# Kernel optimization log

Hardware: AMD Instinct MI355X
Metric: run time of the kernel (lower is better)

## Reference

```python
import jax, jax.numpy as jnp
import numpy as np

B, N, D, H, DK, DV = 16, 512, 512, 8, 64, 64


def setup_inputs() -> dict:
    key = jax.random.key(0)
    ks = jax.random.split(key, 16)
    xav = lambda k, fi, fo: jax.random.uniform(k, (fi, fo), jnp.float32,
                                               -jnp.sqrt(6.0 / (fi + fo)), jnp.sqrt(6.0 / (fi + fo)))
    return {
        "queries": jax.random.normal(ks[0], (B, N, D), jnp.float32),
        "keys": jax.random.normal(ks[1], (B, N, D), jnp.float32),
        "values": jax.random.normal(ks[2], (B, N, D), jnp.float32),
        "box_relation_embed_matrix": jax.random.uniform(ks[3], (B, H, N, N), jnp.float32),
        "ExtrAtt": jax.random.normal(ks[4], (B, H, N, N), jnp.float32),
        "Wq": xav(ks[5], D, H * DK), "bq": jnp.zeros((H * DK,), jnp.float32),
        "Wk": xav(ks[6], D, H * DK), "bk": jnp.zeros((H * DK,), jnp.float32),
        "Wv": xav(ks[7], D, H * DV), "bv": jnp.zeros((H * DV,), jnp.float32),
        "Wo": xav(ks[8], H * DV, D), "bo": jnp.zeros((D,), jnp.float32),
    }


def reference(queries, keys, values, box_relation_embed_matrix, ExtrAtt,
              Wq, bq, Wk, bk, Wv, bv, Wo, bo):
    b_s, nq, _ = queries.shape
    nk = keys.shape[1]
    # projections -> [B, H, N, d]
    q = (queries @ Wq + bq).reshape(b_s, nq, H, DK).transpose(0, 2, 1, 3)
    k = (keys @ Wk + bk).reshape(b_s, nk, H, DK).transpose(0, 2, 1, 3)
    v = (values @ Wv + bv).reshape(b_s, nk, H, DV).transpose(0, 2, 1, 3)
    scale = 1.0 / jnp.sqrt(jnp.asarray(DK, queries.dtype))
    att = jnp.einsum('bhqd,bhkd->bhqk', q, k) * scale
    # log geometric (box) bias + content attention, first softmax
    w_mn = jnp.log(jnp.clip(box_relation_embed_matrix, 1e-6, None)) + att
    w_mn = jax.nn.softmax(w_mn, axis=-1)
    # dropout is identity in eval; add extra attention and re-normalize
    att2 = jax.nn.softmax(w_mn + ExtrAtt, axis=-1)
    out = jnp.einsum('bhqk,bhkd->bhqd', att2, v)
    out = out.transpose(0, 2, 1, 3).reshape(b_s, nq, H * DV)
    return out @ Wo + bo
```

## Files before the change

### kernel.cpp

```cpp
#include <hip/hip_runtime.h>
#include <hip/hip_bf16.h>

#define NB 16
#define NN 512
#define ND 512
#define NH 8

using short8 = __attribute__((ext_vector_type(8))) short;
using f32x4  = __attribute__((ext_vector_type(4))) float;

static __device__ __forceinline__ unsigned short f2bf(float f) {
  unsigned u = __builtin_bit_cast(unsigned, f);
  unsigned r = 0x7fffu + ((u >> 16) & 1u);
  return (unsigned short)((u + r) >> 16);
}
static __device__ __forceinline__ float bf2f(unsigned short u) {
  return __builtin_bit_cast(float, (unsigned)u << 16);
}

__global__ __launch_bounds__(256) void wprep(
    const float* __restrict__ Wq, const float* __restrict__ Wk,
    const float* __restrict__ Wv, const float* __restrict__ Wo,
    unsigned short* __restrict__ T) {
  const float* W;
  switch (blockIdx.z) {
    case 0: W = Wq; break;
    case 1: W = Wk; break;
    case 2: W = Wv; break;
    default: W = Wo; break;
  }
  unsigned short* Wt = T + (size_t)blockIdx.z * 512 * 512;
  __shared__ float tile[64][65];
  const int t = threadIdx.x;
  const int k0 = blockIdx.x * 64, n0 = blockIdx.y * 64;
#pragma unroll
  for (int it = 0; it < 4; ++it) {
    int row = it * 16 + (t >> 4);
    int c4 = (t & 15) * 4;
    float4 v = *(const float4*)&W[(size_t)(k0 + row) * 512 + n0 + c4];
    tile[row][c4] = v.x; tile[row][c4 + 1] = v.y;
    tile[row][c4 + 2] = v.z; tile[row][c4 + 3] = v.w;
  }
  __syncthreads();
#pragma unroll
  for (int it = 0; it < 4; ++it) {
    int nr = it * 16 + (t >> 4);
    int k4 = (t & 15) * 4;
    ushort4 o;
    o.x = f2bf(tile[k4 + 0][nr]); o.y = f2bf(tile[k4 + 1][nr]);
    o.z = f2bf(tile[k4 + 2][nr]); o.w = f2bf(tile[k4 + 3][nr]);
    *(ushort4*)&Wt[(size_t)(n0 + nr) * 512 + k0 + k4] = o;
  }
}

__global__ __launch_bounds__(256) void qkv_gemm(
    const float* __restrict__ Xq, const float* __restrict__ Xk,
    const float* __restrict__ Xv, const unsigned short* __restrict__ Wt,
    const float* __restrict__ bq, const float* __restrict__ bk,
    const float* __restrict__ bv, unsigned short* __restrict__ q_ws,
    unsigned short* __restrict__ k_ws, unsigned short* __restrict__ vt_ws) {
  const int zi = blockIdx.z;
  const float* X = (zi == 0) ? Xq : (zi == 1) ? Xk : Xv;
  const unsigned short* Wz = Wt + (size_t)zi * 512 * 512;
  const float* bias = (zi == 0) ? bq : (zi == 1) ? bk : bv;
  const int m0 = blockIdx.x * 128, n0 = blockIdx.y * 128;
  __shared__ unsigned short Al[2][128][40];
  __shared__ unsigned short Bl[2][128][40];
  const int t = threadIdx.x;
  const int w = t >> 6, l = t & 63;
  const int lr = l & 15, lg = l >> 4;
  const int wr = (w >> 1) * 64, wc = (w & 1) * 64;
  f32x4 acc[4][4] = {};
  for (int kk = 0; kk < 512; kk += 64) {
    __syncthreads();
    {
      const int colk = (t & 15) * 4;
      const int kc = colk >> 5, kin = colk & 31;
#pragma unroll
      for (int p = 0; p < 8; ++p) {
        int row = p * 16 + (t >> 4);
        float4 v = *(const float4*)&X[(size_t)(m0 + row) * 512 + kk + colk];
        ushort4 o;
        o.x = f2bf(v.x); o.y = f2bf(v.y); o.z = f2bf(v.z); o.w = f2bf(v.w);
        *(ushort4*)&Al[kc][row][kin] = o;
      }
      const int colk8 = (t & 7) * 8;
      const int kc2 = colk8 >> 5, kin2 = colk8 & 31;
#pragma unroll
      for (int p = 0; p < 4; ++p) {
        int row = p * 32 + (t >> 3);
        short8 v = *(const short8*)&Wz[(size_t)(n0 + row) * 512 + kk + colk8];
        *(short8*)&Bl[kc2][row][kin2] = v;
      }
    }
    __syncthreads();
#pragma unroll
    for (int kc = 0; kc < 2; ++kc) {
      short8 a[4], b[4];
      const int lk = lg * 8;
#pragma unroll
      for (int i = 0; i < 4; ++i) a[i] = *(const short8*)&Al[kc][wr + i * 16 + lr][lk];
#pragma unroll
      for (int i = 0; i < 4; ++i) b[i] = *(const short8*)&Bl[kc][wc + i * 16 + lr][lk];
#pragma unroll
      for (int i = 0; i < 4; ++i)
#pragma unroll
        for (int j = 0; j < 4; ++j)
          acc[i][j] = __builtin_amdgcn_mfma_f32_16x16x32_bf16(a[i], b[j], acc[i][j], 0, 0, 0);
    }
  }
#pragma unroll
  for (int j = 0; j < 4; ++j) {
    const int col = n0 + wc + j * 16 + lr;
    const float bb = bias[col];
    const int hh = col >> 6, dv = col & 63;
#pragma unroll
    for (int i = 0; i < 4; ++i) {
      const int mbase = m0 + wr + i * 16 + lg * 4;
      const int b_ = mbase >> 9, nt = mbase & 511;
      if (zi == 2) {
        ushort4 o;
        o.x = f2bf(acc[i][j][0] + bb); o.y = f2bf(acc[i][j][1] + bb);
        o.z = f2bf(acc[i][j][2] + bb); o.w = f2bf(acc[i][j][3] + bb);
        *(ushort4*)&vt_ws[((size_t)(b_ * NH + hh) * 64 + dv) * 512 + nt] = o;
      } else {
        unsigned short* dst = (zi == 0) ? q_ws : k_ws;
#pragma unroll
        for (int r = 0; r < 4; ++r)
          dst[((size_t)(b_ * NH + hh) * 512 + nt + r) * 64 + dv] = f2bf(acc[i][j][r] + bb);
      }
    }
  }
}

__global__ __launch_bounds__(256, 8) void attn_kernel(
    const unsigned short* __restrict__ q_ws, const unsigned short* __restrict__ k_ws,
    const unsigned short* __restrict__ vt_ws, const float* __restrict__ box,
    const float* __restrict__ Ext, unsigned short* __restrict__ hidden) {
  const int t = threadIdx.x;
  const int w = t >> 6, l = t & 63;
  const int lr = l & 15, lg = l >> 4;
  const int bh = blockIdx.y;
  const int q0 = blockIdx.x * 16;
  const int b = bh >> 3, h = bh & 7;

  const unsigned short* Qp = q_ws + (size_t)bh * 512 * 64;
  const unsigned short* Kp = k_ws + (size_t)bh * 512 * 64;
  const unsigned short* Vt = vt_ws + (size_t)bh * 64 * 512;
  const float* boxp = box + ((size_t)bh * 512 + q0) * 512;
  const float* Ep = Ext + ((size_t)bh * 512 + q0) * 512;

  __shared__ float red[4][16];
  __shared__ float red2[4][16];
  __shared__ __align__(16) unsigned char wsh[4][4352];

  const int n0w = w * 128;
  unsigned short(*Pw)[136] = (unsigned short(*)[136])wsh[w];

  short8 qf0 = *(const short8*)&Qp[(size_t)(q0 + lr) * 64 + lg * 8];
  short8 qf1 = *(const short8*)&Qp[(size_t)(q0 + lr) * 64 + 32 + lg * 8];

  float s1 = 0.f;
#pragma unroll
  for (int c = 0; c < 8; ++c) {
    const int krow = n0w + c * 16 + lr;
    short8 kf0 = *(const short8*)&Kp[(size_t)krow * 64 + lg * 8];
    short8 kf1 = *(const short8*)&Kp[(size_t)krow * 64 + 32 + lg * 8];
    f32x4 bx4 = *(const f32x4*)&boxp[(size_t)lr * 512 + n0w + c * 16 + lg * 4];
    f32x4 a = {0.f, 0.f, 0.f, 0.f};
    a = __builtin_amdgcn_mfma_f32_16x16x32_bf16(kf0, qf0, a, 0, 0, 0);
    a = __builtin_amdgcn_mfma_f32_16x16x32_bf16(kf1, qf1, a, 0, 0, 0);
    ushort4 o;
    {
      float e0 = fmaxf(bx4[0], 1e-6f) * __expf(a[0] * 0.125f);
      float e1 = fmaxf(bx4[1], 1e-6f) * __expf(a[1] * 0.125f);
      float e2 = fmaxf(bx4[2], 1e-6f) * __expf(a[2] * 0.125f);
      float e3 = fmaxf(bx4[3], 1e-6f) * __expf(a[3] * 0.125f);
      s1 += (e0 + e1) + (e2 + e3);
      o.x = f2bf(e0); o.y = f2bf(e1); o.z = f2bf(e2); o.w = f2bf(e3);
    }
    *(ushort4*)&Pw[lr][c * 16 + lg * 4] = o;
  }
  s1 += __shfl_xor(s1, 16);
  s1 += __shfl_xor(s1, 32);
  if (lg == 0) red[w][lr] = s1;
  __syncthreads();
  const float l1i = 1.0f / (red[0][lr] + red[1][lr] + red[2][lr] + red[3][lr]);

  float s2 = 0.f;
#pragma unroll
  for (int c = 0; c < 8; ++c) {
    f32x4 ex4 = *(const f32x4*)&Ep[(size_t)lr * 512 + n0w + c * 16 + lg * 4];
    ushort4 u = *(const ushort4*)&Pw[lr][c * 16 + lg * 4];
    ushort4 o;
    {
      float e0 = __expf(bf2f(u.x) * l1i + ex4[0]);
      float e1 = __expf(bf2f(u.y) * l1i + ex4[1]);
      float e2 = __expf(bf2f(u.z) * l1i + ex4[2]);
      float e3 = __expf(bf2f(u.w) * l1i + ex4[3]);
      s2 += (e0 + e1) + (e2 + e3);
      o.x = f2bf(e0); o.y = f2bf(e1); o.z = f2bf(e2); o.w = f2bf(e3);
    }
    *(ushort4*)&Pw[lr][c * 16 + lg * 4] = o;
  }
  s2 += __shfl_xor(s2, 16);
  s2 += __shfl_xor(s2, 32);
  if (lg == 0) red2[w][lr] = s2;
  __syncthreads();

  f32x4 o4[4] = {};
#pragma unroll
  for (int kc = 0; kc < 4; ++kc) {
    short8 pa = *(const short8*)&Pw[lr][kc * 32 + lg * 8];
#pragma unroll
    for (int c2 = 0; c2 < 4; ++c2) {
      short8 vf = *(const short8*)&Vt[(size_t)(c2 * 16 + lr) * 512 + n0w + kc * 32 + lg * 8];
      o4[c2] = __builtin_amdgcn_mfma_f32_16x16x32_bf16(pa, vf, o4[c2], 0, 0, 0);
    }
  }
  f32x4 rs = *(const f32x4*)&red2[0][lg * 4];
#pragma unroll
  for (int w2 = 1; w2 < 4; ++w2) {
    f32x4 p = *(const f32x4*)&red2[w2][lg * 4];
#pragma unroll
    for (int r = 0; r < 4; ++r) rs[r] += p[r];
  }
  f32x4 l2v;
#pragma unroll
  for (int r = 0; r < 4; ++r) l2v[r] = 1.0f / rs[r];
  float* ow = (float*)wsh[w];
#pragma unroll
  for (int c2 = 0; c2 < 4; ++c2)
#pragma unroll
    for (int r = 0; r < 4; ++r)
      ow[(lg * 4 + r) * 68 + c2 * 16 + lr] = o4[c2][r] * l2v[r];
  __syncthreads();
  {
    const int lrow = t >> 4;
    const int d4 = (t & 15) * 4;
    f32x4 s = *(const f32x4*)&((const float*)wsh[0])[lrow * 68 + d4];
#pragma unroll
    for (int w2 = 1; w2 < 4; ++w2) {
      f32x4 p = *(const f32x4*)&((const float*)wsh[w2])[lrow * 68 + d4];
#pragma unroll
      for (int r = 0; r < 4; ++r) s[r] += p[r];
    }
    ushort4 oo;
    oo.x = f2bf(s[0]); oo.y = f2bf(s[1]); oo.z = f2bf(s[2]); oo.w = f2bf(s[3]);
    *(ushort4*)&hidden[(size_t)(b * 512 + q0 + lrow) * 512 + h * 64 + d4] = oo;
  }
}

__global__ __launch_bounds__(256) void out_gemm(
    const unsigned short* __restrict__ hidden, const unsigned short* __restrict__ WoT,
    const float* __restrict__ bo, float* __restrict__ out) {
  const int m0 = blockIdx.x * 128, n0 = blockIdx.y * 128;
  __shared__ unsigned short Al[2][128][40];
  __shared__ unsigned short Bl[2][128][40];
  const int t = threadIdx.x;
  const int w = t >> 6, l = t & 63;
  const int lr = l & 15, lg = l >> 4;
  const int wr = (w >> 1) * 64, wc = (w & 1) * 64;
  f32x4 acc[4][4] = {};
  for (int kk = 0; kk < 512; kk += 64) {
    __syncthreads();
    {
      const int colk8 = (t & 7) * 8;
      const int kc2 = colk8 >> 5, kin2 = colk8 & 31;
#pragma unroll
      for (int p = 0; p < 4; ++p) {
        int row = p * 32 + (t >> 3);
        short8 v = *(const short8*)&hidden[(size_t)(m0 + row) * 512 + kk + colk8];
        *(short8*)&Al[kc2][row][kin2] = v;
      }
#pragma unroll
      for (int p = 0; p < 4; ++p) {
        int row = p * 32 + (t >> 3);
        short8 v = *(const short8*)&WoT[(size_t)(n0 + row) * 512 + kk + colk8];
        *(short8*)&Bl[kc2][row][kin2] = v;
      }
    }
    __syncthreads();
#pragma unroll
    for (int kc = 0; kc < 2; ++kc) {
      short8 a[4], b[4];
      const int lk = lg * 8;
#pragma unroll
      for (int i = 0; i < 4; ++i) a[i] = *(const short8*)&Al[kc][wr + i * 16 + lr][lk];
#pragma unroll
      for (int i = 0; i < 4; ++i) b[i] = *(const short8*)&Bl[kc][wc + i * 16 + lr][lk];
#pragma unroll
      for (int i = 0; i < 4; ++i)
#pragma unroll
        for (int j = 0; j < 4; ++j)
          acc[i][j] = __builtin_amdgcn_mfma_f32_16x16x32_bf16(a[i], b[j], acc[i][j], 0, 0, 0);
    }
  }
#pragma unroll
  for (int j = 0; j < 4; ++j) {
    const int col = n0 + wc + j * 16 + lr;
    const float bb = bo[col];
#pragma unroll
    for (int i = 0; i < 4; ++i)
#pragma unroll
      for (int r = 0; r < 4; ++r)
        out[(size_t)(m0 + wr + i * 16 + lg * 4 + r) * 512 + col] = acc[i][j][r] + bb;
  }
}

extern "C" void kernel_launch(void* const* d_in, const int* in_sizes, int n_in,
                              void* d_out, int out_size, void* d_ws, size_t ws_size,
                              hipStream_t stream) {
  const float* queries = (const float*)d_in[0];
  const float* keys = (const float*)d_in[1];
  const float* values = (const float*)d_in[2];
  const float* box = (const float*)d_in[3];
  const float* ext = (const float*)d_in[4];
  const float* Wq = (const float*)d_in[5];
  const float* bq = (const float*)d_in[6];
  const float* Wk = (const float*)d_in[7];
  const float* bk = (const float*)d_in[8];
  const float* Wv = (const float*)d_in[9];
  const float* bv = (const float*)d_in[10];
  const float* Wo = (const float*)d_in[11];
  const float* bo = (const float*)d_in[12];
  float* out = (float*)d_out;

  char* ws = (char*)d_ws;
  unsigned short* q_ws = (unsigned short*)(ws);
  unsigned short* k_ws = (unsigned short*)(ws + 8u * 1024 * 1024);
  unsigned short* vt_ws = (unsigned short*)(ws + 16u * 1024 * 1024);
  unsigned short* hidden = (unsigned short*)(ws + 24u * 1024 * 1024);
  unsigned short* wt = (unsigned short*)(ws + 32u * 1024 * 1024);

  wprep<<<dim3(8, 8, 4), 256, 0, stream>>>(Wq, Wk, Wv, Wo, wt);
  qkv_gemm<<<dim3(64, 4, 3), 256, 0, stream>>>(queries, keys, values, wt, bq, bk, bv,
                                               q_ws, k_ws, vt_ws);
  attn_kernel<<<dim3(32, 128), 256, 0, stream>>>(q_ws, k_ws, vt_ws, box, ext, hidden);
  out_gemm<<<dim3(64, 4), 256, 0, stream>>>(hidden, wt + 3u * 512 * 512, bo, out);
}
```

Measured before the change: 176.5 us.

## Stage box and ExtrAtt tiles into LDS asynchronously, prefetching ExtrAtt during softmax

The attention kernel now copies its box and ExtrAtt tiles from global memory straight into a per-wave, XOR-swizzled LDS buffer with global_load_lds. The ExtrAtt load is issued while the first softmax pass finishes, so its latency overlaps with that compute. All K fragments are loaded up front and the QK MFMAs run before the wait on the box load. Plain __syncthreads is replaced with explicit waitcnt plus s_barrier. In exchange, each block uses roughly 50KB of LDS and launch bounds drop from 8 to 3, so occupancy falls and there is less latency hiding across waves.

```diff
diff --git a/kernel.cpp b/kernel.cpp
--- a/kernel.cpp
+++ b/kernel.cpp
@@ -16,6 +16,10 @@
 }
 static __device__ __forceinline__ float bf2f(unsigned short u) {
   return __builtin_bit_cast(float, (unsigned)u << 16);
+}
+static __device__ __forceinline__ void ld_lds16(const float* g, float* l) {
+  __builtin_amdgcn_global_load_lds((const __attribute__((address_space(1))) void*)g,
+                                   (__attribute__((address_space(3))) void*)l, 16, 0, 0);
 }
 
 __global__ __launch_bounds__(256) void wprep(
@@ -133,7 +137,7 @@
   }
 }
 
-__global__ __launch_bounds__(256, 8) void attn_kernel(
+__global__ __launch_bounds__(256, 3) void attn_kernel(
     const unsigned short* __restrict__ q_ws, const unsigned short* __restrict__ k_ws,
     const unsigned short* __restrict__ vt_ws, const float* __restrict__ box,
     const float* __restrict__ Ext, unsigned short* __restrict__ hidden) {
@@ -150,63 +154,90 @@
   const float* boxp = box + ((size_t)bh * 512 + q0) * 512;
   const float* Ep = Ext + ((size_t)bh * 512 + q0) * 512;
 
+  __shared__ float stg[4][2048];
+  __shared__ unsigned short Pt[4][16][144];
   __shared__ float red[4][16];
   __shared__ float red2[4][16];
-  __shared__ __align__(16) unsigned char wsh[4][4352];
 
   const int n0w = w * 128;
-  unsigned short(*Pw)[136] = (unsigned short(*)[136])wsh[w];
+  float* wst = stg[w];
+  unsigned short(*Pw)[144] = Pt[w];
 
   short8 qf0 = *(const short8*)&Qp[(size_t)(q0 + lr) * 64 + lg * 8];
   short8 qf1 = *(const short8*)&Qp[(size_t)(q0 + lr) * 64 + 32 + lg * 8];
-
-  float s1 = 0.f;
+  short8 kf[8][2];
 #pragma unroll
   for (int c = 0; c < 8; ++c) {
     const int krow = n0w + c * 16 + lr;
-    short8 kf0 = *(const short8*)&Kp[(size_t)krow * 64 + lg * 8];
-    short8 kf1 = *(const short8*)&Kp[(size_t)krow * 64 + 32 + lg * 8];
-    f32x4 bx4 = *(const f32x4*)&boxp[(size_t)lr * 512 + n0w + c * 16 + lg * 4];
+    kf[c][0] = *(const short8*)&Kp[(size_t)krow * 64 + lg * 8];
+    kf[c][1] = *(const short8*)&Kp[(size_t)krow * 64 + 32 + lg * 8];
+  }
+#pragma unroll
+  for (int it = 0; it < 8; ++it) {
+    const int row2 = it * 2 + (l >> 5);
+    const int slot = (l & 31) ^ (row2 & 7);
+    ld_lds16(&boxp[(size_t)row2 * 512 + n0w + slot * 4], &wst[it * 256]);
+  }
+  __builtin_amdgcn_sched_barrier(0);
+
+  f32x4 z[8];
+#pragma unroll
+  for (int c = 0; c < 8; ++c) {
     f32x4 a = {0.f, 0.f, 0.f, 0.f};
-    a = __builtin_amdgcn_mfma_f32_16x16x32_bf16(kf0, qf0, a, 0, 0, 0);
-    a = __builtin_amdgcn_mfma_f32_16x16x32_bf16(kf1, qf1, a, 0, 0, 0);
+    a = __builtin_amdgcn_mfma_f32_16x16x32_bf16(kf[c][0], qf0, a, 0, 0, 0);
+    a = __builtin_amdgcn_mfma_f32_16x16x32_bf16(kf[c][1], qf1, a, 0, 0, 0);
+    z[c] = a;
+  }
+  asm volatile("s_waitcnt vmcnt(0)" ::: "memory");
+
+  float s1 = 0.f;
+#pragma unroll
+  for (int c = 0; c < 8; ++c) {
+    f32x4 bx4 = *(const f32x4*)&wst[lr * 128 + (((c * 4 + lg) ^ (lr & 7)) << 2)];
     ushort4 o;
-    {
-      float e0 = fmaxf(bx4[0], 1e-6f) * __expf(a[0] * 0.125f);
-      float e1 = fmaxf(bx4[1], 1e-6f) * __expf(a[1] * 0.125f);
-      float e2 = fmaxf(bx4[2], 1e-6f) * __expf(a[2] * 0.125f);
-      float e3 = fmaxf(bx4[3], 1e-6f) * __expf(a[3] * 0.125f);
-      s1 += (e0 + e1) + (e2 + e3);
-      o.x = f2bf(e0); o.y = f2bf(e1); o.z = f2bf(e2); o.w = f2bf(e3);
-    }
+    float e0 = fmaxf(bx4[0], 1e-6f) * __expf(z[c][0] * 0.125f);
+    float e1 = fmaxf(bx4[1], 1e-6f) * __expf(z[c][1] * 0.125f);
+    float e2 = fmaxf(bx4[2], 1e-6f) * __expf(z[c][2] * 0.125f);
+    float e3 = fmaxf(bx4[3], 1e-6f) * __expf(z[c][3] * 0.125f);
+    s1 += (e0 + e1) + (e2 + e3);
+    o.x = f2bf(e0); o.y = f2bf(e1); o.z = f2bf(e2); o.w = f2bf(e3);
     *(ushort4*)&Pw[lr][c * 16 + lg * 4] = o;
   }
+  asm volatile("s_waitcnt lgkmcnt(0)" ::: "memory");
+#pragma unroll
+  for (int it = 0; it < 8; ++it) {
+    const int row2 = it * 2 + (l >> 5);
+    const int slot = (l & 31) ^ (row2 & 7);
+    ld_lds16(&Ep[(size_t)row2 * 512 + n0w + slot * 4], &wst[it * 256]);
+  }
+  __builtin_amdgcn_sched_barrier(0);
   s1 += __shfl_xor(s1, 16);
   s1 += __shfl_xor(s1, 32);
   if (lg == 0) red[w][lr] = s1;
-  __syncthreads();
+  asm volatile("s_waitcnt lgkmcnt(0)" ::: "memory");
+  __builtin_amdgcn_s_barrier();
   const float l1i = 1.0f / (red[0][lr] + red[1][lr] + red[2][lr] + red[3][lr]);
+  asm volatile("s_waitcnt vmcnt(0)" ::: "memory");
 
   float s2 = 0.f;
 #pragma unroll
   for (int c = 0; c < 8; ++c) {
-    f32x4 ex4 = *(const f32x4*)&Ep[(size_t)lr * 512 + n0w + c * 16 + lg * 4];
+    f32x4 ex4 = *(const f32x4*)&wst[lr * 128 + (((c * 4 + lg) ^ (lr & 7)) << 2)];
     ushort4 u = *(const ushort4*)&Pw[lr][c * 16 + lg * 4];
     ushort4 o;
-    {
-      float e0 = __expf(bf2f(u.x) * l1i + ex4[0]);
-      float e1 = __expf(bf2f(u.y) * l1i + ex4[1]);
-      float e2 = __expf(bf2f(u.z) * l1i + ex4[2]);
-      float e3 = __expf(bf2f(u.w) * l1i + ex4[3]);
-      s2 += (e0 + e1) + (e2 + e3);
-      o.x = f2bf(e0); o.y = f2bf(e1); o.z = f2bf(e2); o.w = f2bf(e3);
-    }
+    float e0 = __expf(bf2f(u.x) * l1i + ex4[0]);
+    float e1 = __expf(bf2f(u.y) * l1i + ex4[1]);
+    float e2 = __expf(bf2f(u.z) * l1i + ex4[2]);
+    float e3 = __expf(bf2f(u.w) * l1i + ex4[3]);
+    s2 += (e0 + e1) + (e2 + e3);
+    o.x = f2bf(e0); o.y = f2bf(e1); o.z = f2bf(e2); o.w = f2bf(e3);
     *(ushort4*)&Pw[lr][c * 16 + lg * 4] = o;
   }
   s2 += __shfl_xor(s2, 16);
   s2 += __shfl_xor(s2, 32);
   if (lg == 0) red2[w][lr] = s2;
-  __syncthreads();
+  asm volatile("s_waitcnt lgkmcnt(0)" ::: "memory");
+  __builtin_amdgcn_s_barrier();
 
   f32x4 o4[4] = {};
 #pragma unroll
@@ -228,20 +259,21 @@
   f32x4 l2v;
 #pragma unroll
   for (int r = 0; r < 4; ++r) l2v[r] = 1.0f / rs[r];
-  float* ow = (float*)wsh[w];
+  float* ow = (float*)Pw;
 #pragma unroll
   for (int c2 = 0; c2 < 4; ++c2)
 #pragma unroll
     for (int r = 0; r < 4; ++r)
       ow[(lg * 4 + r) * 68 + c2 * 16 + lr] = o4[c2][r] * l2v[r];
-  __syncthreads();
+  asm volatile("s_waitcnt lgkmcnt(0)" ::: "memory");
+  __builtin_amdgcn_s_barrier();
   {
     const int lrow = t >> 4;
     const int d4 = (t & 15) * 4;
-    f32x4 s = *(const f32x4*)&((const float*)wsh[0])[lrow * 68 + d4];
+    f32x4 s = *(const f32x4*)&((const float*)Pt[0])[lrow * 68 + d4];
 #pragma unroll
     for (int w2 = 1; w2 < 4; ++w2) {
-      f32x4 p = *(const f32x4*)&((const float*)wsh[w2])[lrow * 68 + d4];
+      f32x4 p = *(const f32x4*)&((const float*)Pt[w2])[lrow * 68 + d4];
 #pragma unroll
       for (int r = 0; r < 4; ++r) s[r] += p[r];
     }
```

Measured after the change: 157.4 us. 10.8% less time.

## Give each wave a full 16-query row tile, keeping probabilities in registers

Applied to the files above, without the earlier changes.

The attention kernel now assigns one 16-query by full-512-key tile per wave instead of splitting keys across four waves of a block. This removes the shared-memory reductions, block barriers and the cross-wave output reduction. The packed bf16 probabilities stay in registers, and lane shuffles rearrange them into the MFMA A-operand layout for the PV product. The cost is much higher register pressure (64 packed registers per lane) and lower occupancy, with launch bounds lowered to 4. Adjacent waves also now cover different heads at the same query tile, which changes cache locality.

```diff
diff --git a/kernel.cpp b/kernel.cpp
--- a/kernel.cpp
+++ b/kernel.cpp
@@ -8,6 +8,7 @@
 
 using short8 = __attribute__((ext_vector_type(8))) short;
 using f32x4  = __attribute__((ext_vector_type(4))) float;
+using int4v  = __attribute__((ext_vector_type(4))) int;
 
 static __device__ __forceinline__ unsigned short f2bf(float f) {
   unsigned u = __builtin_bit_cast(unsigned, f);
@@ -133,15 +134,16 @@
   }
 }
 
-__global__ __launch_bounds__(256, 8) void attn_kernel(
+__global__ __launch_bounds__(256, 4) void attn_kernel(
     const unsigned short* __restrict__ q_ws, const unsigned short* __restrict__ k_ws,
     const unsigned short* __restrict__ vt_ws, const float* __restrict__ box,
     const float* __restrict__ Ext, unsigned short* __restrict__ hidden) {
   const int t = threadIdx.x;
   const int w = t >> 6, l = t & 63;
   const int lr = l & 15, lg = l >> 4;
-  const int bh = blockIdx.y;
-  const int q0 = blockIdx.x * 16;
+  const int tile = blockIdx.x * 4 + w;
+  const int bh = tile & 127;
+  const int q0 = (tile >> 7) * 16;
   const int b = bh >> 3, h = bh & 7;
 
   const unsigned short* Qp = q_ws + (size_t)bh * 512 * 64;
@@ -150,105 +152,103 @@
   const float* boxp = box + ((size_t)bh * 512 + q0) * 512;
   const float* Ep = Ext + ((size_t)bh * 512 + q0) * 512;
 
-  __shared__ float red[4][16];
-  __shared__ float red2[4][16];
-  __shared__ __align__(16) unsigned char wsh[4][4352];
-
-  const int n0w = w * 128;
-  unsigned short(*Pw)[136] = (unsigned short(*)[136])wsh[w];
-
   short8 qf0 = *(const short8*)&Qp[(size_t)(q0 + lr) * 64 + lg * 8];
   short8 qf1 = *(const short8*)&Qp[(size_t)(q0 + lr) * 64 + 32 + lg * 8];
 
+  unsigned Ppk[32][2];
+
   float s1 = 0.f;
 #pragma unroll
-  for (int c = 0; c < 8; ++c) {
-    const int krow = n0w + c * 16 + lr;
-    short8 kf0 = *(const short8*)&Kp[(size_t)krow * 64 + lg * 8];
-    short8 kf1 = *(const short8*)&Kp[(size_t)krow * 64 + 32 + lg * 8];
-    f32x4 bx4 = *(const f32x4*)&boxp[(size_t)lr * 512 + n0w + c * 16 + lg * 4];
-    f32x4 a = {0.f, 0.f, 0.f, 0.f};
-    a = __builtin_amdgcn_mfma_f32_16x16x32_bf16(kf0, qf0, a, 0, 0, 0);
-    a = __builtin_amdgcn_mfma_f32_16x16x32_bf16(kf1, qf1, a, 0, 0, 0);
-    ushort4 o;
-    {
-      float e0 = fmaxf(bx4[0], 1e-6f) * __expf(a[0] * 0.125f);
-      float e1 = fmaxf(bx4[1], 1e-6f) * __expf(a[1] * 0.125f);
-      float e2 = fmaxf(bx4[2], 1e-6f) * __expf(a[2] * 0.125f);
-      float e3 = fmaxf(bx4[3], 1e-6f) * __expf(a[3] * 0.125f);
+  for (int g = 0; g < 16; ++g) {
+    short8 kf[2][2];
+    f32x4 bx[2];
+#pragma unroll
+    for (int u = 0; u < 2; ++u) {
+      const int c = g * 2 + u;
+      const int krow = c * 16 + lr;
+      kf[u][0] = *(const short8*)&Kp[(size_t)krow * 64 + lg * 8];
+      kf[u][1] = *(const short8*)&Kp[(size_t)krow * 64 + 32 + lg * 8];
+      bx[u] = *(const f32x4*)&boxp[(size_t)lr * 512 + c * 16 + lg * 4];
+    }
+#pragma unroll
+    for (int u = 0; u < 2; ++u) {
+      const int c = g * 2 + u;
+      f32x4 a = {0.f, 0.f, 0.f, 0.f};
+      a = __builtin_amdgcn_mfma_f32_16x16x32_bf16(kf[u][0], qf0, a, 0, 0, 0);
+      a = __builtin_amdgcn_mfma_f32_16x16x32_bf16(kf[u][1], qf1, a, 0, 0, 0);
+      float e0 = fmaxf(bx[u][0], 1e-6f) * __expf(a[0] * 0.125f);
+      float e1 = fmaxf(bx[u][1], 1e-6f) * __expf(a[1] * 0.125f);
+      float e2 = fmaxf(bx[u][2], 1e-6f) * __expf(a[2] * 0.125f);
+      float e3 = fmaxf(bx[u][3], 1e-6f) * __expf(a[3] * 0.125f);
       s1 += (e0 + e1) + (e2 + e3);
-      o.x = f2bf(e0); o.y = f2bf(e1); o.z = f2bf(e2); o.w = f2bf(e3);
-    }
-    *(ushort4*)&Pw[lr][c * 16 + lg * 4] = o;
+      Ppk[c][0] = ((unsigned)f2bf(e1) << 16) | f2bf(e0);
+      Ppk[c][1] = ((unsigned)f2bf(e3) << 16) | f2bf(e2);
+    }
   }
   s1 += __shfl_xor(s1, 16);
   s1 += __shfl_xor(s1, 32);
-  if (lg == 0) red[w][lr] = s1;
-  __syncthreads();
-  const float l1i = 1.0f / (red[0][lr] + red[1][lr] + red[2][lr] + red[3][lr]);
+  const float l1i = 1.0f / s1;
 
   float s2 = 0.f;
 #pragma unroll
-  for (int c = 0; c < 8; ++c) {
-    f32x4 ex4 = *(const f32x4*)&Ep[(size_t)lr * 512 + n0w + c * 16 + lg * 4];
-    ushort4 u = *(const ushort4*)&Pw[lr][c * 16 + lg * 4];
-    ushort4 o;
-    {
-      float e0 = __expf(bf2f(u.x) * l1i + ex4[0]);
-      float e1 = __expf(bf2f(u.y) * l1i + ex4[1]);
-      float e2 = __expf(bf2f(u.z) * l1i + ex4[2]);
-      float e3 = __expf(bf2f(u.w) * l1i + ex4[3]);
-      s2 += (e0 + e1) + (e2 + e3);
-      o.x = f2bf(e0); o.y = f2bf(e1); o.z = f2bf(e2); o.w = f2bf(e3);
-    }
-    *(ushort4*)&Pw[lr][c * 16 + lg * 4] = o;
+  for (int g = 0; g < 8; ++g) {
+    f32x4 ex[4];
+#pragma unroll
+    for (int u = 0; u < 4; ++u)
+      ex[u] = *(const f32x4*)&Ep[(size_t)lr * 512 + (g * 4 + u) * 16 + lg * 4];
+#pragma unroll
+    for (int u = 0; u < 4; ++u) {
+      const int c = g * 4 + u;
+      float p0 = __expf(bf2f((unsigned short)(Ppk[c][0] & 0xffff)) * l1i + ex[u][0]);
+      float p1 = __expf(bf2f((unsigned short)(Ppk[c][0] >> 16)) * l1i + ex[u][1]);
+      float p2 = __expf(bf2f((unsigned short)(Ppk[c][1] & 0xffff)) * l1i + ex[u][2]);
+      float p3 = __expf(bf2f((unsigned short)(Ppk[c][1] >> 16)) * l1i + ex[u][3]);
+      s2 += (p0 + p1) + (p2 + p3);
+      Ppk[c][0] = ((unsigned)f2bf(p1) << 16) | f2bf(p0);
+      Ppk[c][1] = ((unsigned)f2bf(p3) << 16) | f2bf(p2);
+    }
   }
   s2 += __shfl_xor(s2, 16);
   s2 += __shfl_xor(s2, 32);
-  if (lg == 0) red2[w][lr] = s2;
-  __syncthreads();
-
+
+  float l2v[4];
+#pragma unroll
+  for (int r = 0; r < 4; ++r) l2v[r] = 1.0f / __shfl(s2, lg * 4 + r);
+
+  const int src0 = (2 * (lg & 1)) * 16 + lr;
+  const int src1 = src0 + 16;
+  const bool hi = ((lg >> 1) & 1) != 0;
   f32x4 o4[4] = {};
 #pragma unroll
-  for (int kc = 0; kc < 4; ++kc) {
-    short8 pa = *(const short8*)&Pw[lr][kc * 32 + lg * 8];
-#pragma unroll
-    for (int c2 = 0; c2 < 4; ++c2) {
-      short8 vf = *(const short8*)&Vt[(size_t)(c2 * 16 + lr) * 512 + n0w + kc * 32 + lg * 8];
-      o4[c2] = __builtin_amdgcn_mfma_f32_16x16x32_bf16(pa, vf, o4[c2], 0, 0, 0);
-    }
-  }
-  f32x4 rs = *(const f32x4*)&red2[0][lg * 4];
-#pragma unroll
-  for (int w2 = 1; w2 < 4; ++w2) {
-    f32x4 p = *(const f32x4*)&red2[w2][lg * 4];
-#pragma unroll
-    for (int r = 0; r < 4; ++r) rs[r] += p[r];
-  }
-  f32x4 l2v;
-#pragma unroll
-  for (int r = 0; r < 4; ++r) l2v[r] = 1.0f / rs[r];
-  float* ow = (float*)wsh[w];
+  for (int kc = 0; kc < 16; ++kc) {
+    short8 vf[4];
+#pragma unroll
+    for (int c2 = 0; c2 < 4; ++c2)
+      vf[c2] = *(const short8*)&Vt[(size_t)(c2 * 16 + lr) * 512 + kc * 32 + lg * 8];
+    const int a0 = __shfl((int)Ppk[2 * kc][0], src0);
+    const int b0 = __shfl((int)Ppk[2 * kc + 1][0], src0);
+    const int a1 = __shfl((int)Ppk[2 * kc][1], src0);
+    const int b1 = __shfl((int)Ppk[2 * kc + 1][1], src0);
+    const int a2 = __shfl((int)Ppk[2 * kc][0], src1);
+    const int b2 = __shfl((int)Ppk[2 * kc + 1][0], src1);
+    const int a3 = __shfl((int)Ppk[2 * kc][1], src1);
+    const int b3 = __shfl((int)Ppk[2 * kc + 1][1], src1);
+    int4v pu;
+    pu[0] = hi ? b0 : a0;
+    pu[1] = hi ? b1 : a1;
+    pu[2] = hi ? b2 : a2;
+    pu[3] = hi ? b3 : a3;
+    short8 pa = __builtin_bit_cast(short8, pu);
+#pragma unroll
+    for (int c2 = 0; c2 < 4; ++c2)
+      o4[c2] = __builtin_amdgcn_mfma_f32_16x16x32_bf16(pa, vf[c2], o4[c2], 0, 0, 0);
+  }
 #pragma unroll
   for (int c2 = 0; c2 < 4; ++c2)
 #pragma unroll
     for (int r = 0; r < 4; ++r)
-      ow[(lg * 4 + r) * 68 + c2 * 16 + lr] = o4[c2][r] * l2v[r];
-  __syncthreads();
-  {
-    const int lrow = t >> 4;
-    const int d4 = (t & 15) * 4;
-    f32x4 s = *(const f32x4*)&((const float*)wsh[0])[lrow * 68 + d4];
-#pragma unroll
-    for (int w2 = 1; w2 < 4; ++w2) {
-      f32x4 p = *(const f32x4*)&((const float*)wsh[w2])[lrow * 68 + d4];
-#pragma unroll
-      for (int r = 0; r < 4; ++r) s[r] += p[r];
-    }
-    ushort4 oo;
-    oo.x = f2bf(s[0]); oo.y = f2bf(s[1]); oo.z = f2bf(s[2]); oo.w = f2bf(s[3]);
-    *(ushort4*)&hidden[(size_t)(b * 512 + q0 + lrow) * 512 + h * 64 + d4] = oo;
-  }
+      hidden[(size_t)(b * 512 + q0 + lg * 4 + r) * 512 + h * 64 + c2 * 16 + lr] =
+          f2bf(o4[c2][r] * l2v[r]);
 }
 
 __global__ __launch_bounds__(256) void out_gemm(
@@ -336,6 +336,6 @@
   wprep<<<dim3(8, 8, 4), 256, 0, stream>>>(Wq, Wk, Wv, Wo, wt);
   qkv_gemm<<<dim3(64, 4, 3), 256, 0, stream>>>(queries, keys, values, wt, bq, bk, bv,
                                                q_ws, k_ws, vt_ws);
-  attn_kernel<<<dim3(32, 128), 256, 0, stream>>>(q_ws, k_ws, vt_ws, box, ext, hidden);
+  attn_kernel<<<dim3(1024), 256, 0, stream>>>(q_ws, k_ws, vt_ws, box, ext, hidden);
   out_gemm<<<dim3(64, 4), 256, 0, stream>>>(hidden, wt + 3u * 512 * 512, bo, out);
 }
```

Result: no change. 179.3 us (+1.6%).
